# Kernel tuning notes

Measured on AMD Instinct MI355X. Metric: run time of the kernel, lower is better.

Reference implementation:

```python
import jax, jax.numpy as jnp
import numpy as np

EPS = float(np.finfo(np.float32).eps)
SEQ_LEN = 2048
NUM_HEADS = 16
DIM_EMB = 1024
DIM_HEAD = DIM_EMB // NUM_HEADS
DIM_K = DIM_EMB  # module scales by full dim_k, not per-head dim
BATCH = 2


def cosine_positional_encoding(seq_len, dim):
    idx = jnp.arange(seq_len, dtype=jnp.float32)
    scale = 1.0 / (10000.0 ** (jnp.arange(0, dim, 2, dtype=jnp.float32) / dim) + EPS)
    ang = idx[:, None] * scale[None, :]  # [S, dim/2]
    # interleave sin (even) and cos (odd) along last dim -> [S, dim]
    return jnp.stack([jnp.sin(ang), jnp.cos(ang)], axis=-1).reshape(seq_len, dim)


def setup_inputs() -> dict:
    key = jax.random.key(0)
    ks = jax.random.split(key, 5)
    s = DIM_EMB ** -0.5
    return {
        "x": jax.random.normal(ks[0], (BATCH, SEQ_LEN, DIM_EMB), dtype=jnp.float32),
        "Wq": jax.random.normal(ks[1], (DIM_EMB, DIM_EMB), dtype=jnp.float32) * s,
        "Wk": jax.random.normal(ks[2], (DIM_EMB, DIM_EMB), dtype=jnp.float32) * s,
        "Wv": jax.random.normal(ks[3], (DIM_EMB, DIM_EMB), dtype=jnp.float32) * s,
        "Wo": jax.random.normal(ks[4], (DIM_EMB, DIM_EMB), dtype=jnp.float32) * s,
    }


def reference(x, Wq, Wk, Wv, Wo):
    B, S, E = x.shape
    pos = cosine_positional_encoding(S, DIM_HEAD)  # [S, dim_head]
    # projections (bias-free)
    def split_heads(t):
        return t.reshape(B, S, NUM_HEADS, DIM_HEAD).transpose(0, 2, 1, 3)  # [B,H,S,D]
    q = split_heads(x @ Wq) + pos[None, None]
    k = split_heads(x @ Wk) + pos[None, None]
    v = split_heads(x @ Wv)
    scores = jnp.einsum("bhqd,bhkd->bhqk", q, k) * (DIM_K ** -0.5)
    causal_mask = jnp.triu(jnp.ones((S, S), dtype=bool), k=1)
    m_inf = -jnp.finfo(scores.dtype).max
    scores = jnp.where(causal_mask[None, None], m_inf, scores)
    attn = jax.nn.softmax(scores, axis=-1)
    out = jnp.einsum("bhqk,bhkd->bhqd", attn, v)
    out = out.transpose(0, 2, 1, 3).reshape(B, S, E)
    return out @ Wo
```

## Files before the change

kernel.cpp:

```cpp
#include <hip/hip_runtime.h>
#include <math.h>

#define BATCH 2
#define SEQ   2048
#define EMB   1024
#define NHEAD 16
#define DHEAD 64
#define MROWS (BATCH*SEQ)
#define QKS   2048

typedef unsigned int  uint;
typedef unsigned short ushort;
typedef __attribute__((ext_vector_type(8))) short short8;
typedef __attribute__((ext_vector_type(4))) float f32x4;

__device__ __forceinline__ float exp2_fast(float x) {
    return __builtin_amdgcn_exp2f(x);
}

__global__ void pos_init(float* __restrict__ pos) {
    int s = blockIdx.x;
    int d = threadIdx.x;
    int i = d >> 1;
    float expo  = (float)(2 * i) / (float)DHEAD;
    float scale = 1.0f / (powf(10000.0f, expo) + 1.1920928955078125e-07f);
    float ang   = (float)s * scale;
    pos[s * DHEAD + d] = (d & 1) ? cosf(ang) : sinf(ang);
}

__device__ __forceinline__ uint pack_bf16x2(float a, float b) {
    union { float f; uint u; } x, y;
    x.f = a; y.f = b;
    uint ua = x.u + 0x7fffu + ((x.u >> 16) & 1u);
    uint ub = y.u + 0x7fffu + ((y.u >> 16) & 1u);
    return (ua >> 16) | (ub & 0xffff0000u);
}
__device__ __forceinline__ ushort bf16_1(float a) {
    union { float f; uint u; } x; x.f = a;
    return (ushort)((x.u + 0x7fffu + ((x.u >> 16) & 1u)) >> 16);
}

__device__ __forceinline__ void gll16(const ushort* g, ushort* l) {
    __builtin_amdgcn_global_load_lds(
        (const __attribute__((address_space(1))) uint*)g,
        (__attribute__((address_space(3))) uint*)l, 16, 0, 0);
}

__global__ __launch_bounds__(256) void cvt_bf16(
    const float* __restrict__ in, ushort* __restrict__ out, int n2) {
    int gid = blockIdx.x * 256 + threadIdx.x;
    if (gid < n2) {
        float2 v = ((const float2*)in)[gid];
        ((uint*)out)[gid] = pack_bf16x2(v.x, v.y);
    }
}

__global__ __launch_bounds__(256) void wt_bf16_all(
    const float* __restrict__ Wq, const float* __restrict__ Wk,
    const float* __restrict__ Wv, const float* __restrict__ Wo,
    ushort* __restrict__ Wqkvt, ushort* __restrict__ Wot) {
    __shared__ float tile[32][33];
    const int which = blockIdx.z;
    const float* W = (which == 0) ? Wq : (which == 1) ? Wk : (which == 2) ? Wv : Wo;
    ushort* Wt = (which < 3) ? (Wqkvt + (size_t)which * 1024 * EMB) : Wot;
    const int c0 = blockIdx.x * 32;
    const int r0 = blockIdx.y * 32;
    const int tx = threadIdx.x & 31;
    const int ty = threadIdx.x >> 5;
#pragma unroll
    for (int i = 0; i < 4; ++i)
        tile[ty + i * 8][tx] = W[(size_t)(r0 + ty + i * 8) * EMB + c0 + tx];
    __syncthreads();
#pragma unroll
    for (int i = 0; i < 4; ++i)
        Wt[(size_t)(c0 + ty + i * 8) * EMB + r0 + tx] = bf16_1(tile[tx][ty + i * 8]);
}

#define TK 32
#define SCLQ (0.03125f * 1.44269504088896f)

template<int TMT>
__global__ __launch_bounds__(256) void gemm_mfma_t(
    const ushort* __restrict__ A, const ushort* __restrict__ Bt,
    void* __restrict__ Cv, ushort* __restrict__ VtOut,
    const float* __restrict__ pos, int posmode, int N, int K) {
    constexpr int MI = TMT / 32;
    __shared__ ushort As[TMT * TK];
    __shared__ ushort Bs[128 * TK];

    const int t    = threadIdx.x;
    const int lane = t & 63, w = t >> 6;
    const int quad = lane >> 4, l15 = lane & 15;
    const int bm = blockIdx.x * TMT, bn = blockIdx.y * 128;
    const int wm = (w & 1) * (TMT / 2), wn = (w >> 1) * 64;
    const int r0 = t >> 2, kp = (t & 3) * 8;

    f32x4 acc[MI][4];
#pragma unroll
    for (int mi = 0; mi < MI; ++mi)
#pragma unroll
        for (int ni = 0; ni < 4; ++ni)
            acc[mi][ni] = (f32x4){0.f, 0.f, 0.f, 0.f};

    for (int k0 = 0; k0 < K; k0 += TK) {
        __syncthreads();
#pragma unroll
        for (int i = 0; i < TMT / 64; ++i)
            gll16(A + (size_t)(bm + i * 64 + r0) * K + k0 + kp, &As[i * 2048 + t * 8]);
#pragma unroll
        for (int i = 0; i < 2; ++i)
            gll16(Bt + (size_t)(bn + i * 64 + r0) * K + k0 + kp, &Bs[i * 2048 + t * 8]);
        __syncthreads();

        short8 af[MI], bfv[4];
#pragma unroll
        for (int mi = 0; mi < MI; ++mi)
            af[mi] = *(const short8*)&As[(wm + mi * 16 + l15) * TK + quad * 8];
#pragma unroll
        for (int ni = 0; ni < 4; ++ni)
            bfv[ni] = *(const short8*)&Bs[(wn + ni * 16 + l15) * TK + quad * 8];
#pragma unroll
        for (int mi = 0; mi < MI; ++mi)
#pragma unroll
            for (int ni = 0; ni < 4; ++ni)
                acc[mi][ni] = __builtin_amdgcn_mfma_f32_16x16x32_bf16(
                    af[mi], bfv[ni], acc[mi][ni], 0, 0, 0);
    }

#pragma unroll
    for (int mi = 0; mi < MI; ++mi) {
        const int row0 = bm + wm + mi * 16 + quad * 4;
#pragma unroll
        for (int ni = 0; ni < 4; ++ni) {
            const int col = bn + wn + ni * 16 + l15;
            if (!posmode) {
#pragma unroll
                for (int r = 0; r < 4; ++r)
                    ((float*)Cv)[(size_t)(row0 + r) * N + col] = acc[mi][ni][r];
            } else if (col < 2048) {
#pragma unroll
                for (int r = 0; r < 4; ++r) {
                    const int row = row0 + r;
                    const int s   = row & (SEQ - 1);
                    float v = acc[mi][ni][r] + pos[s * DHEAD + (col & 63)];
                    if (col < 1024) v *= SCLQ;
                    ((ushort*)Cv)[(size_t)row * QKS + col] = bf16_1(v);
                }
            } else {
                const int hh = (col >> 6) & 15;
                const int d  = col & 63;
                const int bb = row0 >> 11;
                const int s0 = row0 & (SEQ - 1);
                uint2 u;
                u.x = pack_bf16x2(acc[mi][ni][0], acc[mi][ni][1]);
                u.y = pack_bf16x2(acc[mi][ni][2], acc[mi][ni][3]);
                *(uint2*)&VtOut[((size_t)(bb * 16 + hh) * 64 + d) * SEQ + s0] = u;
            }
        }
    }
}

#define LDP 72

__device__ __forceinline__ void rd_frags(
    const ushort* __restrict__ S, short8 (&f0)[4], short8 (&f1)[4],
    int quad, int l15) {
#pragma unroll
    for (int g = 0; g < 4; ++g) {
        f0[g] = *(const short8*)&S[(g * 16 + l15) * LDP + quad * 8];
        f1[g] = *(const short8*)&S[(g * 16 + l15) * LDP + 32 + quad * 8];
    }
}

template<bool DIAG>
__device__ __forceinline__ void qk_tile(
    const short8 (&ak0)[4], const short8 (&ak1)[4],
    short8 aq0, short8 aq1, float (&sv)[4][4], float& pmax,
    int keyb0, int qrow, int quad) {
#pragma unroll
    for (int kg = 0; kg < 4; ++kg) {
        f32x4 a = (f32x4){0.f, 0.f, 0.f, 0.f};
        a = __builtin_amdgcn_mfma_f32_16x16x32_bf16(ak0[kg], aq0, a, 0, 0, 0);
        a = __builtin_amdgcn_mfma_f32_16x16x32_bf16(ak1[kg], aq1, a, 0, 0, 0);
        const int keyb = keyb0 + kg * 16 + quad * 4;
#pragma unroll
        for (int r = 0; r < 4; ++r) {
            float v = a[r];
            if (DIAG && (keyb + r > qrow)) v = -3.0e38f;
            sv[kg][r] = v;
            pmax = fmaxf(pmax, v);
        }
    }
}

__device__ __forceinline__ void sm_pv(
    float (&sv)[4][4], float& m_l, float& l_l, float pmax,
    f32x4 (&acc)[4], ushort* __restrict__ Pw,
    const short8 (&bv0)[4], const short8 (&bv1)[4], int quad, int l15) {
    pmax = fmaxf(pmax, __shfl_xor(pmax, 16, 64));
    pmax = fmaxf(pmax, __shfl_xor(pmax, 32, 64));
    if (__any(pmax - m_l > 8.f)) {
        const float m_new = fmaxf(m_l, pmax);
        const float alpha = exp2_fast(m_l - m_new);
        m_l = m_new;
        l_l *= alpha;
        float av[4];
#pragma unroll
        for (int r = 0; r < 4; ++r) av[r] = __shfl(alpha, quad * 4 + r, 64);
#pragma unroll
        for (int nd = 0; nd < 4; ++nd)
#pragma unroll
            for (int r = 0; r < 4; ++r) acc[nd][r] *= av[r];
    }
    float rs = 0.f;
#pragma unroll
    for (int kg = 0; kg < 4; ++kg)
#pragma unroll
        for (int r = 0; r < 4; ++r) {
            float p = exp2_fast(sv[kg][r] - m_l);
            sv[kg][r] = p;
            rs += p;
        }
    rs += __shfl_xor(rs, 16, 64);
    rs += __shfl_xor(rs, 32, 64);
    l_l += rs;
#pragma unroll
    for (int kg = 0; kg < 4; ++kg) {
        uint2 u;
        u.x = pack_bf16x2(sv[kg][0], sv[kg][1]);
        u.y = pack_bf16x2(sv[kg][2], sv[kg][3]);
        *(uint2*)&Pw[l15 * LDP + kg * 16 + quad * 4] = u;
    }
    const short8 pa0 = *(const short8*)&Pw[l15 * LDP + quad * 8];
    const short8 pa1 = *(const short8*)&Pw[l15 * LDP + 32 + quad * 8];
#pragma unroll
    for (int nd = 0; nd < 4; ++nd) {
        acc[nd] = __builtin_amdgcn_mfma_f32_16x16x32_bf16(pa0, bv0[nd], acc[nd], 0, 0, 0);
        acc[nd] = __builtin_amdgcn_mfma_f32_16x16x32_bf16(pa1, bv1[nd], acc[nd], 0, 0, 0);
    }
}

__global__ __launch_bounds__(256, 2) void attn_mfma10(
    const ushort* __restrict__ QK, const ushort* __restrict__ Vt,
    ushort* __restrict__ AOb) {
    __shared__ ushort Ks[2][64 * LDP];
    __shared__ ushort Vs[2][64 * LDP];
    __shared__ ushort Ps[2][64 * LDP];

    const int bid  = blockIdx.x;
    const int bh   = (bid & 7) | (((bid >> 7) & 3) << 3);
    const int pair = (bid >> 3) & 15;
    const int b    = bh >> 4, hd = bh & 15;
    const int t    = threadIdx.x;
    const int lane = t & 63, w = t >> 6;
    const int quad = lane >> 4, l15 = lane & 15;
    const int wrow = w * 16;
    const int sr = t >> 2;
    const int sc = (t & 3) * 16;

    const int qtA = pair;
    const int qtB = 31 - pair;

    const size_t qkbase = (size_t)b * SEQ * QKS + hd * 64;
    const ushort* kpb = QK + qkbase + 1024 + (size_t)sr * QKS + sc;
    const ushort* vpb = Vt + ((size_t)bh * 64 + sr) * SEQ;

    const ushort* qpA = QK + qkbase + (size_t)(qtA * 64 + wrow + l15) * QKS + quad * 8;
    const short8 aqA0 = *(const short8*)qpA;
    const short8 aqA1 = *(const short8*)(qpA + 32);
    const ushort* qpB = QK + qkbase + (size_t)(qtB * 64 + wrow + l15) * QKS + quad * 8;
    const short8 aqB0 = *(const short8*)qpB;
    const short8 aqB1 = *(const short8*)(qpB + 32);

    uint4 ka = *(const uint4*)kpb;
    uint4 kb = *(const uint4*)(kpb + 8);
    uint4 va = *(const uint4*)(vpb + sc);
    uint4 vb = *(const uint4*)(vpb + sc + 8);
    int cur = 0;

    f32x4 accA[4], accB[4];
#pragma unroll
    for (int nd = 0; nd < 4; ++nd) {
        accA[nd] = (f32x4){0.f, 0.f, 0.f, 0.f};
        accB[nd] = (f32x4){0.f, 0.f, 0.f, 0.f};
    }
    float mA = -3.0e38f, lA = 0.f, mB = -3.0e38f, lB = 0.f;
    const int qrowA = qtA * 64 + wrow + l15;
    const int qrowB = qtB * 64 + wrow + l15;
    ushort* PwA = &Ps[0][wrow * LDP];
    ushort* PwB = &Ps[1][wrow * LDP];

    for (int kt = 0; kt <= qtB; ++kt) {
        ushort* Kc = Ks[cur];
        ushort* Vc = Vs[cur];
        *(uint4*)&Kc[sr * LDP + sc]     = ka;
        *(uint4*)&Kc[sr * LDP + sc + 8] = kb;
        *(uint4*)&Vc[sr * LDP + sc]     = va;
        *(uint4*)&Vc[sr * LDP + sc + 8] = vb;
        const int ktn = (kt < qtB) ? kt + 1 : qtB;
        ka = *(const uint4*)(kpb + (size_t)ktn * 64 * QKS);
        kb = *(const uint4*)(kpb + (size_t)ktn * 64 * QKS + 8);
        va = *(const uint4*)(vpb + ktn * 64 + sc);
        vb = *(const uint4*)(vpb + ktn * 64 + sc + 8);
        __syncthreads();

        short8 ak0[4], ak1[4];
        rd_frags(Kc, ak0, ak1, quad, l15);

        const bool actA = (kt <= qtA);
        const int keyb0 = kt * 64;

        float svB[4][4]; float pmB = -3.0e38f;
        if (kt == qtB) qk_tile<true >(ak0, ak1, aqB0, aqB1, svB, pmB, keyb0, qrowB, quad);
        else           qk_tile<false>(ak0, ak1, aqB0, aqB1, svB, pmB, keyb0, qrowB, quad);

        float svA[4][4]; float pmA = -3.0e38f;
        if (actA) {
            if (kt == qtA) qk_tile<true >(ak0, ak1, aqA0, aqA1, svA, pmA, keyb0, qrowA, quad);
            else           qk_tile<false>(ak0, ak1, aqA0, aqA1, svA, pmA, keyb0, qrowA, quad);
        }

        short8 bv0[4], bv1[4];
        rd_frags(Vc, bv0, bv1, quad, l15);

        sm_pv(svB, mB, lB, pmB, accB, PwB, bv0, bv1, quad, l15);
        if (actA) sm_pv(svA, mA, lA, pmA, accA, PwA, bv0, bv1, quad, l15);

        cur ^= 1;
    }

    {
        float linv[4];
#pragma unroll
        for (int r = 0; r < 4; ++r) linv[r] = 1.0f / __shfl(lB, quad * 4 + r, 64);
#pragma unroll
        for (int nd = 0; nd < 4; ++nd)
#pragma unroll
            for (int r = 0; r < 4; ++r) {
                const int row = qtB * 64 + wrow + quad * 4 + r;
                AOb[(size_t)(b * SEQ + row) * EMB + hd * 64 + nd * 16 + l15] =
                    bf16_1(accB[nd][r] * linv[r]);
            }
    }
    {
        float linv[4];
#pragma unroll
        for (int r = 0; r < 4; ++r) linv[r] = 1.0f / __shfl(lA, quad * 4 + r, 64);
#pragma unroll
        for (int nd = 0; nd < 4; ++nd)
#pragma unroll
            for (int r = 0; r < 4; ++r) {
                const int row = qtA * 64 + wrow + quad * 4 + r;
                AOb[(size_t)(b * SEQ + row) * EMB + hd * 64 + nd * 16 + l15] =
                    bf16_1(accA[nd][r] * linv[r]);
            }
    }
}

#define BM 64
#define BN 64
#define BK 16

__global__ __launch_bounds__(256) void gemm_f32(
    const float* __restrict__ A, const float* __restrict__ B,
    float* __restrict__ C, const float* __restrict__ pos, int addpos,
    int M, int N, int K) {
    __shared__ float As[BK][BM];
    __shared__ float Bs[BK][BN];
    const int tid = threadIdx.x;
    const int bm  = blockIdx.x * BM;
    const int bn  = blockIdx.y * BN;
    const int tx  = tid & 15;
    const int ty  = tid >> 4;
    const int arow = tid >> 2;
    const int acol = (tid & 3) << 2;
    const int brow = tid >> 4;
    const int bcol = (tid & 15) << 2;
    float acc[4][4] = {{0.f}};
    const float* Aptr = A + (size_t)(bm + arow) * K + acol;
    const float* Bptr = B + (size_t)brow * N + bn + bcol;
    for (int k0 = 0; k0 < K; k0 += BK) {
        float4 av = *(const float4*)(Aptr + k0);
        float4 bv = *(const float4*)(Bptr + (size_t)k0 * N);
        __syncthreads();
        As[acol + 0][arow] = av.x;
        As[acol + 1][arow] = av.y;
        As[acol + 2][arow] = av.z;
        As[acol + 3][arow] = av.w;
        *(float4*)&Bs[brow][bcol] = bv;
        __syncthreads();
#pragma unroll
        for (int kk = 0; kk < BK; ++kk) {
            float4 a = *(const float4*)&As[kk][ty << 2];
            float4 b = *(const float4*)&Bs[kk][tx << 2];
            float aa[4] = {a.x, a.y, a.z, a.w};
            float bb[4] = {b.x, b.y, b.z, b.w};
#pragma unroll
            for (int i = 0; i < 4; ++i)
#pragma unroll
                for (int j = 0; j < 4; ++j)
                    acc[i][j] += aa[i] * bb[j];
        }
    }
#pragma unroll
    for (int i = 0; i < 4; ++i) {
        int m = bm + (ty << 2) + i;
        int n = bn + (tx << 2);
        float4 v = make_float4(acc[i][0], acc[i][1], acc[i][2], acc[i][3]);
        if (addpos) {
            int s = m & (SEQ - 1);
            int d = n & (DHEAD - 1);
            float4 p = *(const float4*)&pos[s * DHEAD + d];
            v.x += p.x; v.y += p.y; v.z += p.z; v.w += p.w;
        }
        *(float4*)&C[(size_t)m * N + n] = v;
    }
}

#define QT 128
#define KT 32
__global__ __launch_bounds__(QT) void attn_fwd(
    const float* __restrict__ Q, const float* __restrict__ Kg,
    const float* __restrict__ V, float* __restrict__ O) {
    __shared__ float Ks[KT][DHEAD];
    __shared__ float Vs[KT][DHEAD];
    const int t    = threadIdx.x;
    const int q0   = blockIdx.x * QT;
    const int bh   = blockIdx.y;
    const int b    = bh >> 4;
    const int h    = bh & 15;
    const int qrow = q0 + t;
    const size_t base = (size_t)b * SEQ * EMB + (size_t)h * DHEAD;
    float4 q4[16], o4[16];
#pragma unroll
    for (int i = 0; i < 16; ++i) {
        q4[i] = *(const float4*)&Q[base + (size_t)qrow * EMB + i * 4];
        o4[i] = make_float4(0.f, 0.f, 0.f, 0.f);
    }
    float m_i = -3.0e38f, l_i = 0.0f;
    const float scale = 0.03125f;
    const int kend = q0 + QT;
    for (int k0 = 0; k0 < kend; k0 += KT) {
        __syncthreads();
#pragma unroll
        for (int i = 0; i < 4; ++i) {
            int idx = t + i * QT;
            int r = idx >> 4;
            int c = (idx & 15) << 2;
            *(float4*)&Ks[r][c] = *(const float4*)&Kg[base + (size_t)(k0 + r) * EMB + c];
            *(float4*)&Vs[r][c] = *(const float4*)&V [base + (size_t)(k0 + r) * EMB + c];
        }
        __syncthreads();
        float sv[KT];
        float mt = m_i;
#pragma unroll
        for (int j = 0; j < KT; ++j) {
            const float4* kr = (const float4*)Ks[j];
            float dot = 0.f;
#pragma unroll
            for (int dd = 0; dd < 16; ++dd) {
                float4 kv = kr[dd];
                dot += q4[dd].x * kv.x + q4[dd].y * kv.y +
                       q4[dd].z * kv.z + q4[dd].w * kv.w;
            }
            sv[j] = (k0 + j <= qrow) ? dot * scale : -3.0e38f;
            mt = fmaxf(mt, sv[j]);
        }
        float corr = __expf(m_i - mt);
        l_i *= corr;
#pragma unroll
        for (int i = 0; i < 16; ++i) {
            o4[i].x *= corr; o4[i].y *= corr; o4[i].z *= corr; o4[i].w *= corr;
        }
#pragma unroll
        for (int j = 0; j < KT; ++j) {
            float pp = __expf(sv[j] - mt);
            l_i += pp;
            const float4* vr = (const float4*)Vs[j];
#pragma unroll
            for (int dd = 0; dd < 16; ++dd) {
                float4 vv = vr[dd];
                o4[dd].x += pp * vv.x; o4[dd].y += pp * vv.y;
                o4[dd].z += pp * vv.z; o4[dd].w += pp * vv.w;
            }
        }
        m_i = mt;
    }
    float inv = 1.0f / l_i;
#pragma unroll
    for (int i = 0; i < 16; ++i) {
        float4 v = o4[i];
        v.x *= inv; v.y *= inv; v.z *= inv; v.w *= inv;
        *(float4*)&O[base + (size_t)qrow * EMB + i * 4] = v;
    }
}

extern "C" void kernel_launch(void* const* d_in, const int* in_sizes, int n_in,
                              void* d_out, int out_size, void* d_ws, size_t ws_size,
                              hipStream_t stream) {
    const float* x  = (const float*)d_in[0];
    const float* Wq = (const float*)d_in[1];
    const float* Wk = (const float*)d_in[2];
    const float* Wv = (const float*)d_in[3];
    const float* Wo = (const float*)d_in[4];
    float* out = (float*)d_out;

    char* ws = (char*)d_ws;
    size_t off = 0;
    float*  pos   = (float*)(ws + off);  off += (size_t)SEQ * DHEAD * 4;
    ushort* xb    = (ushort*)(ws + off); off += (size_t)MROWS * EMB * 2;
    ushort* Wqkvt = (ushort*)(ws + off); off += (size_t)3072 * EMB * 2;
    ushort* Wot   = (ushort*)(ws + off); off += (size_t)EMB * EMB * 2;
    ushort* QKb   = (ushort*)(ws + off); off += (size_t)MROWS * QKS * 2;
    ushort* Vtp   = (ushort*)(ws + off); off += (size_t)MROWS * EMB * 2;
    ushort* AOb   = (ushort*)(ws + off); off += (size_t)MROWS * EMB * 2;
    const bool use_bf16 = off <= ws_size;

    const int M = MROWS, K = EMB;

    pos_init<<<SEQ, DHEAD, 0, stream>>>(pos);

    if (use_bf16) {
        const int n2 = MROWS * EMB / 2;
        cvt_bf16<<<n2 / 256, 256, 0, stream>>>(x, xb, n2);
        wt_bf16_all<<<dim3(EMB / 32, EMB / 32, 4), 256, 0, stream>>>(
            Wq, Wk, Wv, Wo, Wqkvt, Wot);

        gemm_mfma_t<128><<<dim3(M / 128, 3072 / 128), 256, 0, stream>>>(
            xb, Wqkvt, QKb, Vtp, pos, 1, 3072, K);

        attn_mfma10<<<dim3(512), 256, 0, stream>>>(QKb, Vtp, AOb);

        gemm_mfma_t<64><<<dim3(M / 64, EMB / 128), 256, 0, stream>>>(
            AOb, Wot, out, nullptr, pos, 0, EMB, K);
    } else {
        size_t f = 0;
        float* posf = (float*)(ws + f); f += (size_t)SEQ * DHEAD * 4;
        float* Qb = (float*)(ws + f); f += (size_t)MROWS * EMB * 4;
        float* Kb = (float*)(ws + f); f += (size_t)MROWS * EMB * 4;
        float* Vb = (float*)(ws + f); f += (size_t)MROWS * EMB * 4;
        float* AO = (float*)(ws + f);
        dim3 g(M / BM, EMB / BN);
        gemm_f32<<<g, 256, 0, stream>>>(x, Wq, Qb, posf, 1, M, EMB, K);
        gemm_f32<<<g, 256, 0, stream>>>(x, Wk, Kb, posf, 1, M, EMB, K);
        gemm_f32<<<g, 256, 0, stream>>>(x, Wv, Vb, posf, 0, M, EMB, K);
        attn_fwd<<<dim3(SEQ / QT, BATCH * NHEAD), QT, 0, stream>>>(Qb, Kb, Vb, AO);
        gemm_f32<<<g, 256, 0, stream>>>(AO, Wo, out, posf, 0, M, EMB, K);
    }
}
```

Before: 190.7 us.

## Merge prep kernels into one launch, tree-reduce softmax, reorder prefetch after barrier

Folds the x conversion, weight transpose/convert, and positional-encoding init into a single prep_all launch, removing two kernel launches. It swaps the hand-written bf16 rounding for HIP intrinsics. In attention, the per-tile max and row sum become short trees instead of serial chains to shorten dependency latency. The next-tile global prefetch now sits after the barrier, which changes how load latency overlaps with the sync.

```diff
diff --git a/kernel.cpp b/kernel.cpp
--- a/kernel.cpp
+++ b/kernel.cpp
@@ -1,4 +1,5 @@
 #include <hip/hip_runtime.h>
+#include <hip/hip_bf16.h>
 #include <math.h>
 
 #define BATCH 2
@@ -16,6 +17,21 @@
 
 __device__ __forceinline__ float exp2_fast(float x) {
     return __builtin_amdgcn_exp2f(x);
+}
+
+__device__ __forceinline__ uint pack_bf16x2(float a, float b) {
+    __hip_bfloat162 h = __float22bfloat162_rn(make_float2(a, b));
+    return *reinterpret_cast<uint*>(&h);
+}
+__device__ __forceinline__ ushort bf16_1(float a) {
+    __hip_bfloat16 h = __float2bfloat16(a);
+    return *reinterpret_cast<ushort*>(&h);
+}
+
+__device__ __forceinline__ void gll16(const ushort* g, ushort* l) {
+    __builtin_amdgcn_global_load_lds(
+        (const __attribute__((address_space(1))) uint*)g,
+        (__attribute__((address_space(3))) uint*)l, 16, 0, 0);
 }
 
 __global__ void pos_init(float* __restrict__ pos) {
@@ -28,52 +44,45 @@
     pos[s * DHEAD + d] = (d & 1) ? cosf(ang) : sinf(ang);
 }
 
-__device__ __forceinline__ uint pack_bf16x2(float a, float b) {
-    union { float f; uint u; } x, y;
-    x.f = a; y.f = b;
-    uint ua = x.u + 0x7fffu + ((x.u >> 16) & 1u);
-    uint ub = y.u + 0x7fffu + ((y.u >> 16) & 1u);
-    return (ua >> 16) | (ub & 0xffff0000u);
-}
-__device__ __forceinline__ ushort bf16_1(float a) {
-    union { float f; uint u; } x; x.f = a;
-    return (ushort)((x.u + 0x7fffu + ((x.u >> 16) & 1u)) >> 16);
-}
-
-__device__ __forceinline__ void gll16(const ushort* g, ushort* l) {
-    __builtin_amdgcn_global_load_lds(
-        (const __attribute__((address_space(1))) uint*)g,
-        (__attribute__((address_space(3))) uint*)l, 16, 0, 0);
-}
-
-__global__ __launch_bounds__(256) void cvt_bf16(
-    const float* __restrict__ in, ushort* __restrict__ out, int n2) {
-    int gid = blockIdx.x * 256 + threadIdx.x;
-    if (gid < n2) {
-        float2 v = ((const float2*)in)[gid];
-        ((uint*)out)[gid] = pack_bf16x2(v.x, v.y);
-    }
-}
-
-__global__ __launch_bounds__(256) void wt_bf16_all(
+__global__ __launch_bounds__(256) void prep_all(
+    const float* __restrict__ x,
     const float* __restrict__ Wq, const float* __restrict__ Wk,
     const float* __restrict__ Wv, const float* __restrict__ Wo,
-    ushort* __restrict__ Wqkvt, ushort* __restrict__ Wot) {
+    ushort* __restrict__ xb, ushort* __restrict__ Wqkvt,
+    ushort* __restrict__ Wot, float* __restrict__ pos) {
     __shared__ float tile[32][33];
-    const int which = blockIdx.z;
-    const float* W = (which == 0) ? Wq : (which == 1) ? Wk : (which == 2) ? Wv : Wo;
-    ushort* Wt = (which < 3) ? (Wqkvt + (size_t)which * 1024 * EMB) : Wot;
-    const int c0 = blockIdx.x * 32;
-    const int r0 = blockIdx.y * 32;
-    const int tx = threadIdx.x & 31;
-    const int ty = threadIdx.x >> 5;
-#pragma unroll
-    for (int i = 0; i < 4; ++i)
-        tile[ty + i * 8][tx] = W[(size_t)(r0 + ty + i * 8) * EMB + c0 + tx];
-    __syncthreads();
-#pragma unroll
-    for (int i = 0; i < 4; ++i)
-        Wt[(size_t)(c0 + ty + i * 8) * EMB + r0 + tx] = bf16_1(tile[tx][ty + i * 8]);
+    const int bid = blockIdx.x;
+    if (bid < 8192) {
+        int gid = bid * 256 + threadIdx.x;
+        float2 v = ((const float2*)x)[gid];
+        ((uint*)xb)[gid] = pack_bf16x2(v.x, v.y);
+    } else if (bid < 8192 + 4096) {
+        const int wb    = bid - 8192;
+        const int which = wb >> 10;
+        const int inner = wb & 1023;
+        const float* W = (which == 0) ? Wq : (which == 1) ? Wk
+                       : (which == 2) ? Wv : Wo;
+        ushort* Wt = (which < 3) ? (Wqkvt + (size_t)which * 1024 * EMB) : Wot;
+        const int c0 = (inner & 31) * 32;
+        const int r0 = (inner >> 5) * 32;
+        const int tx = threadIdx.x & 31;
+        const int ty = threadIdx.x >> 5;
+#pragma unroll
+        for (int i = 0; i < 4; ++i)
+            tile[ty + i * 8][tx] = W[(size_t)(r0 + ty + i * 8) * EMB + c0 + tx];
+        __syncthreads();
+#pragma unroll
+        for (int i = 0; i < 4; ++i)
+            Wt[(size_t)(c0 + ty + i * 8) * EMB + r0 + tx] = bf16_1(tile[tx][ty + i * 8]);
+    } else {
+        const int idx = (bid - 12288) * 256 + threadIdx.x;
+        const int s = idx >> 6, d = idx & 63;
+        const int i = d >> 1;
+        float expo  = (float)(2 * i) / (float)DHEAD;
+        float scale = 1.0f / (powf(10000.0f, expo) + 1.1920928955078125e-07f);
+        float ang   = (float)s * scale;
+        pos[s * DHEAD + d] = (d & 1) ? cosf(ang) : sinf(ang);
+    }
 }
 
 #define TK 32
@@ -188,8 +197,10 @@
             float v = a[r];
             if (DIAG && (keyb + r > qrow)) v = -3.0e38f;
             sv[kg][r] = v;
-            pmax = fmaxf(pmax, v);
-        }
+        }
+        const float m01 = fmaxf(sv[kg][0], sv[kg][1]);
+        const float m23 = fmaxf(sv[kg][2], sv[kg][3]);
+        pmax = fmaxf(pmax, fmaxf(m01, m23));
     }
 }
 
@@ -214,13 +225,14 @@
     }
     float rs = 0.f;
 #pragma unroll
-    for (int kg = 0; kg < 4; ++kg)
+    for (int kg = 0; kg < 4; ++kg) {
 #pragma unroll
         for (int r = 0; r < 4; ++r) {
             float p = exp2_fast(sv[kg][r] - m_l);
             sv[kg][r] = p;
-            rs += p;
-        }
+        }
+        rs += (sv[kg][0] + sv[kg][1]) + (sv[kg][2] + sv[kg][3]);
+    }
     rs += __shfl_xor(rs, 16, 64);
     rs += __shfl_xor(rs, 32, 64);
     l_l += rs;
@@ -240,7 +252,7 @@
     }
 }
 
-__global__ __launch_bounds__(256, 2) void attn_mfma10(
+__global__ __launch_bounds__(256, 2) void attn_mfma11(
     const ushort* __restrict__ QK, const ushort* __restrict__ Vt,
     ushort* __restrict__ AOb) {
     __shared__ ushort Ks[2][64 * LDP];
@@ -297,12 +309,13 @@
         *(uint4*)&Kc[sr * LDP + sc + 8] = kb;
         *(uint4*)&Vc[sr * LDP + sc]     = va;
         *(uint4*)&Vc[sr * LDP + sc + 8] = vb;
+        __syncthreads();
+
         const int ktn = (kt < qtB) ? kt + 1 : qtB;
         ka = *(const uint4*)(kpb + (size_t)ktn * 64 * QKS);
         kb = *(const uint4*)(kpb + (size_t)ktn * 64 * QKS + 8);
         va = *(const uint4*)(vpb + ktn * 64 + sc);
         vb = *(const uint4*)(vpb + ktn * 64 + sc + 8);
-        __syncthreads();
 
         short8 ak0[4], ak1[4];
         rd_frags(Kc, ak0, ak1, quad, l15);
@@ -518,18 +531,14 @@
 
     const int M = MROWS, K = EMB;
 
-    pos_init<<<SEQ, DHEAD, 0, stream>>>(pos);
-
     if (use_bf16) {
-        const int n2 = MROWS * EMB / 2;
-        cvt_bf16<<<n2 / 256, 256, 0, stream>>>(x, xb, n2);
-        wt_bf16_all<<<dim3(EMB / 32, EMB / 32, 4), 256, 0, stream>>>(
-            Wq, Wk, Wv, Wo, Wqkvt, Wot);
+        prep_all<<<dim3(12800), 256, 0, stream>>>(
+            x, Wq, Wk, Wv, Wo, xb, Wqkvt, Wot, pos);
 
         gemm_mfma_t<128><<<dim3(M / 128, 3072 / 128), 256, 0, stream>>>(
             xb, Wqkvt, QKb, Vtp, pos, 1, 3072, K);
 
-        attn_mfma10<<<dim3(512), 256, 0, stream>>>(QKb, Vtp, AOb);
+        attn_mfma11<<<dim3(512), 256, 0, stream>>>(QKb, Vtp, AOb);
 
         gemm_mfma_t<64><<<dim3(M / 64, EMB / 128), 256, 0, stream>>>(
             AOb, Wot, out, nullptr, pos, 0, EMB, K);
@@ -540,6 +549,7 @@
         float* Kb = (float*)(ws + f); f += (size_t)MROWS * EMB * 4;
         float* Vb = (float*)(ws + f); f += (size_t)MROWS * EMB * 4;
         float* AO = (float*)(ws + f);
+        pos_init<<<SEQ, DHEAD, 0, stream>>>(posf);
         dim3 g(M / BM, EMB / BN);
         gemm_f32<<<g, 256, 0, stream>>>(x, Wq, Qb, posf, 1, M, EMB, K);
         gemm_f32<<<g, 256, 0, stream>>>(x, Wk, Kb, posf, 1, M, EMB, K);
```

New measurement: 188.5 us. About the same (-1.2%).
